# Optimization experiments

Hardware: AMD Instinct MI355X
Metric: run time of the kernel (lower is better)

Reference implementation:

```python
import jax, jax.numpy as jnp
import numpy as np

B, T, D, H = 4, 2048, 512, 8
DH = D // H  # 64
EPS = 1e-5


def setup_inputs() -> dict:
    key = jax.random.key(0)
    ks = jax.random.split(key, 12)
    s = lambda k, shp, fan: jax.random.normal(k, shp, jnp.float32) * (fan ** -0.5)
    return {
        "x": jax.random.normal(ks[0], (B, T, D), jnp.float32),
        "ln1_g": jnp.ones((D,), jnp.float32),
        "ln1_b": jnp.zeros((D,), jnp.float32),
        "Wq": s(ks[1], (H, D, DH), D),  # per-head bias-free projections
        "Wk": s(ks[2], (H, D, DH), D),
        "Wv": s(ks[3], (H, D, DH), D),
        "Wproj": s(ks[4], (D, D), D),
        "bproj": jnp.zeros((D,), jnp.float32),
        "W1": s(ks[5], (D, 4 * D), D),
        "b1": jnp.zeros((4 * D,), jnp.float32),
        "W2": s(ks[6], (4 * D, D), 4 * D),
        "b2": jnp.zeros((D,), jnp.float32),
    }


def _layernorm(x, g, b):
    m = jnp.mean(x, axis=-1, keepdims=True)
    v = jnp.var(x, axis=-1, keepdims=True)
    return (x - m) * jax.lax.rsqrt(v + EPS) * g + b


def reference(x, ln1_g, ln1_b, Wq, Wk, Wv, Wproj, bproj, W1, b1, W2, b2):
    b, t, c = x.shape
    scale = c ** -0.5  # source scales by input channel dim, not head_size
    causal = jnp.tril(jnp.ones((t, t), bool))  # [T,T]

    # --- attention sublayer (pre-norm with ln1) ---
    h = _layernorm(x, ln1_g, ln1_b)
    q = jnp.einsum('btd,hde->bhte', h, Wq)
    k = jnp.einsum('btd,hde->bhte', h, Wk)
    v = jnp.einsum('btd,hde->bhte', h, Wv)
    scores = jnp.einsum('bhte,bhse->bhts', q, k) * scale  # [B,H,T,T]
    scores = jnp.where(causal, scores, -jnp.inf)
    att = jax.nn.softmax(scores, axis=-1)  # dropout = identity at inference
    o = jnp.einsum('bhts,bhse->bthe', att, v).reshape(b, t, c)  # concat heads
    sa = o @ Wproj + bproj
    x = x + sa

    # --- FFN sublayer (source reuses ln1, faithful) ---
    h2 = _layernorm(x, ln1_g, ln1_b)
    ff = jax.nn.relu(h2 @ W1 + b1) @ W2 + b2
    return x + ff
```

## Files before the change

### kernel.cpp

```cpp
#include <hip/hip_runtime.h>
#include <math.h>

#define B_ 4
#define T_ 2048
#define D_ 512
#define H_ 8
#define DH_ 64
#define BT_ 8192
#define FF_ 2048
#define EPS_ 1e-5f
#define SCALE_ 0.04419417382415922f
#define SC2_ 0.06375861151f
#define NEGINF_ -1e30f

typedef short b16x8 __attribute__((ext_vector_type(8)));
typedef short b16x4 __attribute__((ext_vector_type(4)));
typedef float f32x4 __attribute__((ext_vector_type(4)));

#define MFMA16(a, b, c) __builtin_amdgcn_mfma_f32_16x16x32_bf16(a, b, c, 0, 0, 0)
#define MFMA16K16(a, b, c) __builtin_amdgcn_mfma_f32_16x16x16bf16_1k(a, b, c, 0, 0, 0)

#define GLL16(gp, lp) \
    __builtin_amdgcn_global_load_lds((const __attribute__((address_space(1))) void*)(gp), \
                                     (__attribute__((address_space(3))) void*)(lp), 16, 0, 0)

#if __has_builtin(__builtin_amdgcn_exp2f)
#define EXP2F(x) __builtin_amdgcn_exp2f(x)
#else
#define EXP2F(x) exp2f(x)
#endif

static __device__ inline short f2bf(float f) {
    unsigned int u = __builtin_bit_cast(unsigned int, f);
    unsigned int r = (u + 0x7fffu + ((u >> 16) & 1u)) >> 16;
    return (short)r;
}
static __device__ inline short f2bf_trunc(float f) {
    return (short)(__builtin_bit_cast(unsigned int, f) >> 16);
}

__global__ __launch_bounds__(64) void ln_kernel(const float* __restrict__ X,
        const float* __restrict__ G, const float* __restrict__ Bb,
        short* __restrict__ Y)
{
    int row = blockIdx.x;
    int t = threadIdx.x;
    const float* xr = X + (size_t)row * D_;
    float4 v0 = *(const float4*)(xr + t * 4);
    float4 v1 = *(const float4*)(xr + 256 + t * 4);
    float sum = v0.x + v0.y + v0.z + v0.w + v1.x + v1.y + v1.z + v1.w;
    float ssq = v0.x*v0.x + v0.y*v0.y + v0.z*v0.z + v0.w*v0.w
              + v1.x*v1.x + v1.y*v1.y + v1.z*v1.z + v1.w*v1.w;
    #pragma unroll
    for (int off = 32; off > 0; off >>= 1) {
        sum += __shfl_down(sum, off);
        ssq += __shfl_down(ssq, off);
    }
    sum = __shfl(sum, 0);
    ssq = __shfl(ssq, 0);
    float mean = sum * (1.0f / D_);
    float var  = ssq * (1.0f / D_) - mean * mean;
    float rstd = rsqrtf(var + EPS_);

    float4 g0 = *(const float4*)(G + t * 4);
    float4 g1 = *(const float4*)(G + 256 + t * 4);
    float4 b0 = *(const float4*)(Bb + t * 4);
    float4 b1 = *(const float4*)(Bb + 256 + t * 4);
    short4 o0, o1;
    o0.x = f2bf((v0.x - mean) * rstd * g0.x + b0.x);
    o0.y = f2bf((v0.y - mean) * rstd * g0.y + b0.y);
    o0.z = f2bf((v0.z - mean) * rstd * g0.z + b0.z);
    o0.w = f2bf((v0.w - mean) * rstd * g0.w + b0.w);
    o1.x = f2bf((v1.x - mean) * rstd * g1.x + b1.x);
    o1.y = f2bf((v1.y - mean) * rstd * g1.y + b1.y);
    o1.z = f2bf((v1.z - mean) * rstd * g1.z + b1.z);
    o1.w = f2bf((v1.w - mean) * rstd * g1.w + b1.w);
    short* yr = Y + (size_t)row * D_;
    *(short4*)(yr + t * 4)       = o0;
    *(short4*)(yr + 256 + t * 4) = o1;
}

__global__ __launch_bounds__(256) void prep_kernel(
        const float* __restrict__ Wq, const float* __restrict__ Wk,
        const float* __restrict__ Wv, const float* __restrict__ Wp,
        const float* __restrict__ W1, const float* __restrict__ W2,
        short* __restrict__ wqkv, short* __restrict__ wpt,
        short* __restrict__ w1t, short* __restrict__ w2t)
{
    __shared__ float tile[32][33];
    int idx = blockIdx.x;
    const float* src; short* dst; int R, C, tx0, ty0;
    if (idx < 768) {
        int w = idx >> 8, rem = idx & 255;
        int hh = rem >> 5, t = rem & 31;
        const float* base = (w == 0) ? Wq : ((w == 1) ? Wk : Wv);
        src = base + hh * (D_ * DH_);
        dst = wqkv + w * (512 * 512) + hh * (DH_ * D_);
        R = 512; C = 64; tx0 = (t & 1) * 32; ty0 = (t >> 1) * 32;
    } else if (idx < 1024) {
        int t = idx - 768;
        src = Wp; dst = wpt; R = 512; C = 512;
        tx0 = (t & 15) * 32; ty0 = (t >> 4) * 32;
    } else if (idx < 2048) {
        int t = idx - 1024;
        src = W1; dst = w1t; R = 512; C = 2048;
        tx0 = (t & 63) * 32; ty0 = (t >> 6) * 32;
    } else {
        int t = idx - 2048;
        src = W2; dst = w2t; R = 2048; C = 512;
        tx0 = (t & 15) * 32; ty0 = (t >> 4) * 32;
    }
    int tx = threadIdx.x, ty = threadIdx.y;
    #pragma unroll
    for (int i = 0; i < 32; i += 8)
        tile[ty + i][tx] = src[(size_t)(ty0 + ty + i) * C + tx0 + tx];
    __syncthreads();
    #pragma unroll
    for (int i = 0; i < 32; i += 8)
        dst[(size_t)(tx0 + ty + i) * R + ty0 + tx] = f2bf(tile[tx][ty + i]);
}

__global__ __launch_bounds__(256) void mm_kernel(const short* __restrict__ A,
        const short* __restrict__ Bt, void* __restrict__ C,
        const float* __restrict__ bias, const float* __restrict__ resid,
        int M, int N, int K, int relu, int out_bf16)
{
    __shared__ short As[2][128 * 32];
    __shared__ short Bs[2][128 * 32];
    const int tid = threadIdx.x;
    const int wave = tid >> 6, lane = tid & 63;
    const int quad = lane >> 4, l15 = lane & 15;
    const int m0 = blockIdx.x * 128, n0 = blockIdx.y * 128;
    const int mw = (wave & 1) * 64, nw = (wave >> 1) * 64;

#define STAGE_MM(bufi, kk) \
    { \
        for (int r = 0; r < 2; ++r) { \
            int c = r * 256 + tid; \
            int row = c >> 2, seg = (c & 3) ^ (row & 3); \
            GLL16(A + (size_t)(m0 + row) * K + (kk) + seg * 8, \
                  As[bufi] + (size_t)(r * 256 + wave * 64) * 8); \
            GLL16(Bt + (size_t)(n0 + row) * K + (kk) + seg * 8, \
                  Bs[bufi] + (size_t)(r * 256 + wave * 64) * 8); \
        } \
    }

    f32x4 acc[4][4];
    #pragma unroll
    for (int i = 0; i < 4; ++i)
        #pragma unroll
        for (int j = 0; j < 4; ++j)
            acc[i][j] = (f32x4){0.f, 0.f, 0.f, 0.f};

    STAGE_MM(0, 0);
    int buf = 0;
    for (int k0 = 0; k0 < K; k0 += 32) {
        __syncthreads();
        if (k0 + 32 < K) STAGE_MM(buf ^ 1, k0 + 32);
        b16x8 af[4], bf[4];
        #pragma unroll
        for (int i = 0; i < 4; ++i) {
            int row = mw + i * 16 + l15;
            af[i] = *(const b16x8*)(As[buf] + row * 32 + ((quad ^ (row & 3)) * 8));
        }
        #pragma unroll
        for (int j = 0; j < 4; ++j) {
            int row = nw + j * 16 + l15;
            bf[j] = *(const b16x8*)(Bs[buf] + row * 32 + ((quad ^ (row & 3)) * 8));
        }
        #pragma unroll
        for (int i = 0; i < 4; ++i)
            #pragma unroll
            for (int j = 0; j < 4; ++j)
                acc[i][j] = MFMA16(af[i], bf[j], acc[i][j]);
        buf ^= 1;
    }
#undef STAGE_MM

    #pragma unroll
    for (int i = 0; i < 4; ++i) {
        #pragma unroll
        for (int r = 0; r < 4; ++r) {
            size_t row = (size_t)(m0 + mw + i * 16 + quad * 4 + r);
            #pragma unroll
            for (int j = 0; j < 4; ++j) {
                int col = n0 + nw + j * 16 + l15;
                float v = acc[i][j][r];
                if (bias)  v += bias[col];
                if (resid) v += resid[row * N + col];
                if (relu)  v = fmaxf(v, 0.0f);
                if (out_bf16) ((short*)C)[row * N + col] = f2bf(v);
                else          ((float*)C)[row * N + col] = v;
            }
        }
    }
}

__global__ __launch_bounds__(256) void mm64_kernel(const short* __restrict__ A,
        const short* __restrict__ Bt, void* __restrict__ C,
        const float* __restrict__ bias, const float* __restrict__ resid,
        int M, int N, int K, int relu, int out_bf16)
{
    __shared__ short As[2][128 * 32];
    __shared__ short Bs[2][64 * 32];
    const int tid = threadIdx.x;
    const int wave = tid >> 6, lane = tid & 63;
    const int quad = lane >> 4, l15 = lane & 15;
    const int m0 = blockIdx.x * 128, n0 = blockIdx.y * 64;
    const int mw = (wave & 1) * 64, nw = (wave >> 1) * 32;

#define STAGE_M64(bufi, kk) \
    { \
        for (int r = 0; r < 2; ++r) { \
            int c = r * 256 + tid; \
            int row = c >> 2, seg = (c & 3) ^ (row & 3); \
            GLL16(A + (size_t)(m0 + row) * K + (kk) + seg * 8, \
                  As[bufi] + (size_t)(r * 256 + wave * 64) * 8); \
        } \
        { \
            int row = tid >> 2, seg = (tid & 3) ^ (row & 3); \
            GLL16(Bt + (size_t)(n0 + row) * K + (kk) + seg * 8, \
                  Bs[bufi] + (size_t)(wave * 64) * 8); \
        } \
    }

    f32x4 acc[4][2];
    #pragma unroll
    for (int i = 0; i < 4; ++i)
        #pragma unroll
        for (int j = 0; j < 2; ++j)
            acc[i][j] = (f32x4){0.f, 0.f, 0.f, 0.f};

    STAGE_M64(0, 0);
    int buf = 0;
    for (int k0 = 0; k0 < K; k0 += 32) {
        __syncthreads();
        if (k0 + 32 < K) STAGE_M64(buf ^ 1, k0 + 32);
        b16x8 af[4], bf[2];
        #pragma unroll
        for (int i = 0; i < 4; ++i) {
            int row = mw + i * 16 + l15;
            af[i] = *(const b16x8*)(As[buf] + row * 32 + ((quad ^ (row & 3)) * 8));
        }
        #pragma unroll
        for (int j = 0; j < 2; ++j) {
            int row = nw + j * 16 + l15;
            bf[j] = *(const b16x8*)(Bs[buf] + row * 32 + ((quad ^ (row & 3)) * 8));
        }
        #pragma unroll
        for (int i = 0; i < 4; ++i)
            #pragma unroll
            for (int j = 0; j < 2; ++j)
                acc[i][j] = MFMA16(af[i], bf[j], acc[i][j]);
        buf ^= 1;
    }
#undef STAGE_M64

    #pragma unroll
    for (int i = 0; i < 4; ++i) {
        #pragma unroll
        for (int r = 0; r < 4; ++r) {
            size_t row = (size_t)(m0 + mw + i * 16 + quad * 4 + r);
            #pragma unroll
            for (int j = 0; j < 2; ++j) {
                int col = n0 + nw + j * 16 + l15;
                float v = acc[i][j][r];
                if (bias)  v += bias[col];
                if (resid) v += resid[row * N + col];
                if (relu)  v = fmaxf(v, 0.0f);
                if (out_bf16) ((short*)C)[row * N + col] = f2bf(v);
                else          ((float*)C)[row * N + col] = v;
            }
        }
    }
}

__global__ __launch_bounds__(256) void mm6464_kernel(const short* __restrict__ A,
        const short* __restrict__ Bt, void* __restrict__ C,
        const float* __restrict__ bias, const float* __restrict__ resid,
        int M, int N, int K, int relu, int out_bf16)
{
    __shared__ short As[2][64 * 32];
    __shared__ short Bs[2][64 * 32];
    const int tid = threadIdx.x;
    const int wave = tid >> 6, lane = tid & 63;
    const int quad = lane >> 4, l15 = lane & 15;
    const int m0 = blockIdx.x * 64, n0 = blockIdx.y * 64;
    const int nw = wave * 16;

#define STAGE_M66(bufi, kk) \
    { \
        int row = tid >> 2, seg = (tid & 3) ^ (row & 3); \
        GLL16(A + (size_t)(m0 + row) * K + (kk) + seg * 8, \
              As[bufi] + (size_t)(wave * 64) * 8); \
        GLL16(Bt + (size_t)(n0 + row) * K + (kk) + seg * 8, \
              Bs[bufi] + (size_t)(wave * 64) * 8); \
    }

    f32x4 acc[4];
    #pragma unroll
    for (int i = 0; i < 4; ++i) acc[i] = (f32x4){0.f, 0.f, 0.f, 0.f};

    STAGE_M66(0, 0);
    int buf = 0;
    for (int k0 = 0; k0 < K; k0 += 32) {
        __syncthreads();
        if (k0 + 32 < K) STAGE_M66(buf ^ 1, k0 + 32);
        b16x8 af[4], bf;
        #pragma unroll
        for (int i = 0; i < 4; ++i) {
            int row = i * 16 + l15;
            af[i] = *(const b16x8*)(As[buf] + row * 32 + ((quad ^ (row & 3)) * 8));
        }
        {
            int row = nw + l15;
            bf = *(const b16x8*)(Bs[buf] + row * 32 + ((quad ^ (row & 3)) * 8));
        }
        #pragma unroll
        for (int i = 0; i < 4; ++i)
            acc[i] = MFMA16(af[i], bf, acc[i]);
        buf ^= 1;
    }
#undef STAGE_M66

    #pragma unroll
    for (int i = 0; i < 4; ++i) {
        #pragma unroll
        for (int r = 0; r < 4; ++r) {
            size_t row = (size_t)(m0 + i * 16 + quad * 4 + r);
            int col = n0 + nw + l15;
            float v = acc[i][r];
            if (bias)  v += bias[col];
            if (resid) v += resid[row * N + col];
            if (relu)  v = fmaxf(v, 0.0f);
            if (out_bf16) ((short*)C)[row * N + col] = f2bf(v);
            else          ((float*)C)[row * N + col] = v;
        }
    }
}

__global__ __launch_bounds__(256) void attn_kernel(const short* __restrict__ qkv,
        short* __restrict__ Ob)
{
    __shared__ short Qs[64 * 64];
    __shared__ short Ks[64 * 64];
    __shared__ short Vt[64 * 64];
    __shared__ short Osh[64 * 72];

    const int tid = threadIdx.x;
    const int wave = tid >> 6, lane = tid & 63;
    const int quad = lane >> 4, l15 = lane & 15;
    const int bh = blockIdx.x;
    const int qi = 31 - (int)blockIdx.y;
    const int b = bh >> 3, h = bh & 7;
    const size_t tok0 = (size_t)b * T_;
    const int qrow_rel = wave * 16 + l15;

    #pragma unroll
    for (int r = 0; r < 2; ++r) {
        int c = r * 256 + tid;
        int tk = c >> 3;
        int seg = (c & 7) ^ (tk & 7);
        GLL16(qkv + (tok0 + qi * 64 + tk) * 1536 + h * 64 + seg * 8,
              Qs + (size_t)(r * 256 + wave * 64) * 8);
    }

    float mrow = NEGINF_, lrow = 0.0f;
    f32x4 ot[4];
    #pragma unroll
    for (int dt = 0; dt < 4; ++dt) ot[dt] = (f32x4){0.f, 0.f, 0.f, 0.f};

    b16x8 qf[2];

    for (int kj = 0; kj <= qi; ++kj) {
        __syncthreads();
        #pragma unroll
        for (int r = 0; r < 2; ++r) {
            int c = r * 256 + tid;
            int tk = c >> 3;
            int seg = (c & 7) ^ (tk & 7);
            GLL16(qkv + (tok0 + kj * 64 + tk) * 1536 + 512 + h * 64 + seg * 8,
                  Ks + (size_t)(r * 256 + wave * 64) * 8);
        }
        {
            int s = tid >> 5, tp = tid & 31;
            const short* g0 = qkv + (tok0 + kj * 64 + tp * 2) * 1536 + 1024 + h * 64 + s * 8;
            b16x8 v0 = *(const b16x8*)g0;
            b16x8 v1 = *(const b16x8*)(g0 + 1536);
            int* vo = (int*)Vt;
            int gg = tp >> 1, half = tp & 1;
            #pragma unroll
            for (int e = 0; e < 8; ++e) {
                int row = s * 8 + e;
                unsigned int pk = (unsigned int)(unsigned short)v0[e]
                                | ((unsigned int)(unsigned short)v1[e] << 16);
                vo[row * 32 + ((gg ^ (row & 15)) << 1) + half] = pk;
            }
        }
        __syncthreads();

        if (kj == 0) {
            #pragma unroll
            for (int kb = 0; kb < 2; ++kb) {
                int row = wave * 16 + l15;
                qf[kb] = *(const b16x8*)(Qs + row * 64 + (((kb * 4 + quad) ^ (row & 7)) * 8));
            }
        }

        f32x4 st[4];
        #pragma unroll
        for (int mt = 0; mt < 4; ++mt) st[mt] = (f32x4){0.f, 0.f, 0.f, 0.f};
        #pragma unroll
        for (int mt = 0; mt < 4; ++mt) {
            int trow = mt * 16 + l15;
            #pragma unroll
            for (int kb = 0; kb < 2; ++kb) {
                b16x8 kf = *(const b16x8*)(Ks + trow * 64 + (((kb * 4 + quad) ^ (trow & 7)) * 8));
                st[mt] = MFMA16(kf, qf[kb], st[mt]);
            }
        }

        const bool diag = (kj == qi);
        float mx = NEGINF_;
        #pragma unroll
        for (int mt = 0; mt < 4; ++mt)
            #pragma unroll
            for (int r = 0; r < 4; ++r) {
                if (diag && (mt * 16 + quad * 4 + r) > qrow_rel) st[mt][r] = NEGINF_;
                mx = fmaxf(mx, st[mt][r]);
            }
        mx = fmaxf(mx, __shfl_xor(mx, 16));
        mx = fmaxf(mx, __shfl_xor(mx, 32));
        float mn = fmaxf(mrow, mx);
        float alpha = EXP2F((mrow - mn) * SC2_);
        float mnsc = mn * SC2_;
        mrow = mn;
        float rs = 0.0f;
        b16x4 pf[4];
        #pragma unroll
        for (int mt = 0; mt < 4; ++mt)
            #pragma unroll
            for (int r = 0; r < 4; ++r) {
                float e = EXP2F(fmaf(st[mt][r], SC2_, -mnsc));
                rs += e;
                pf[mt][r] = f2bf_trunc(e);
            }
        rs += __shfl_xor(rs, 16);
        rs += __shfl_xor(rs, 32);
        lrow = lrow * alpha + rs;
        #pragma unroll
        for (int dt = 0; dt < 4; ++dt) {
            ot[dt][0] *= alpha; ot[dt][1] *= alpha;
            ot[dt][2] *= alpha; ot[dt][3] *= alpha;
        }
        #pragma unroll
        for (int dt = 0; dt < 4; ++dt) {
            const short* vrow = Vt + (dt * 16 + l15) * 64;
            #pragma unroll
            for (int kt = 0; kt < 4; ++kt) {
                b16x4 vf = *(const b16x4*)(vrow + (((kt * 4 + quad) ^ l15) << 2));
                ot[dt] = MFMA16K16(vf, pf[kt], ot[dt]);
            }
        }
    }

    float inv = 1.0f / lrow;
    #pragma unroll
    for (int dt = 0; dt < 4; ++dt) {
        b16x4 o4;
        o4[0] = f2bf(ot[dt][0] * inv);
        o4[1] = f2bf(ot[dt][1] * inv);
        o4[2] = f2bf(ot[dt][2] * inv);
        o4[3] = f2bf(ot[dt][3] * inv);
        *(b16x4*)(Osh + (size_t)qrow_rel * 72 + dt * 16 + quad * 4) = o4;
    }
    {
        int row = tid >> 2, ch = tid & 3;
        b16x8 lo = *(const b16x8*)(Osh + (size_t)row * 72 + ch * 16);
        b16x8 hi = *(const b16x8*)(Osh + (size_t)row * 72 + ch * 16 + 8);
        short* dst = Ob + (tok0 + (size_t)qi * 64 + row) * 512 + h * 64 + ch * 16;
        *(b16x8*)dst = lo;
        *(b16x8*)(dst + 8) = hi;
    }
}

extern "C" void kernel_launch(void* const* d_in, const int* in_sizes, int n_in,
                              void* d_out, int out_size, void* d_ws, size_t ws_size,
                              hipStream_t stream) {
    (void)in_sizes; (void)n_in; (void)out_size; (void)ws_size;
    const float* x     = (const float*)d_in[0];
    const float* ln_g  = (const float*)d_in[1];
    const float* ln_b  = (const float*)d_in[2];
    const float* Wq    = (const float*)d_in[3];
    const float* Wk    = (const float*)d_in[4];
    const float* Wv    = (const float*)d_in[5];
    const float* Wproj = (const float*)d_in[6];
    const float* bproj = (const float*)d_in[7];
    const float* W1    = (const float*)d_in[8];
    const float* b1    = (const float*)d_in[9];
    const float* W2    = (const float*)d_in[10];
    const float* b2    = (const float*)d_in[11];
    float* out = (float*)d_out;

    char* W = (char*)d_ws;
    short* hbuf  = (short*)(W + 0);
    short* qkvb  = (short*)(W + ((size_t)8  << 20));
    short* attno = (short*)(W + ((size_t)32 << 20));
    float* x1    = (float*)(W + ((size_t)40 << 20));
    short* ff1   = (short*)(W + ((size_t)56 << 20));
    short* wqkv  = (short*)(W + ((size_t)88 << 20));
    short* wpt   = (short*)(W + ((size_t)90 << 20));
    short* w1t   = (short*)(W + ((size_t)91 << 20));
    short* w2t   = (short*)(W + ((size_t)93 << 20));

    prep_kernel<<<dim3(3072), dim3(32, 8), 0, stream>>>(
        Wq, Wk, Wv, Wproj, W1, W2, wqkv, wpt, w1t, w2t);
    ln_kernel<<<dim3(BT_), dim3(64), 0, stream>>>(x, ln_g, ln_b, hbuf);
    mm_kernel<<<dim3(64, 12), dim3(256), 0, stream>>>(hbuf, wqkv, qkvb,
        nullptr, nullptr, BT_, 1536, D_, 0, 1);
    attn_kernel<<<dim3(32, 32), dim3(256), 0, stream>>>(qkvb, attno);
    mm6464_kernel<<<dim3(128, 8), dim3(256), 0, stream>>>(attno, wpt, x1,
        bproj, x, BT_, D_, D_, 0, 0);
    ln_kernel<<<dim3(BT_), dim3(64), 0, stream>>>(x1, ln_g, ln_b, hbuf);
    mm_kernel<<<dim3(64, 16), dim3(256), 0, stream>>>(hbuf, w1t, ff1,
        b1, nullptr, BT_, FF_, D_, 1, 1);
    mm64_kernel<<<dim3(64, 8), dim3(256), 0, stream>>>(ff1, w2t, out,
        b2, x1, BT_, D_, FF_, 0, 0);
}
```

Before: 294.5 us.

## Split attention KV range in two and merge partials in a combine kernel

The attention kernel now splits each query tile's causal key range into two halves across a new grid dimension. Each half writes a normalized bf16 partial output and per-row max/sum to workspace, and a new combine kernel merges the two with log-sum-exp weights. This targets load imbalance and low block count from the triangular causal loop. In exchange it adds an extra launch, extra global traffic for the partials, and an additional bf16 rounding of the partial outputs.

```diff
diff --git a/kernel.cpp b/kernel.cpp
--- a/kernel.cpp
+++ b/kernel.cpp
@@ -37,6 +37,9 @@
 }
 static __device__ inline short f2bf_trunc(float f) {
     return (short)(__builtin_bit_cast(unsigned int, f) >> 16);
+}
+static __device__ inline float bf2f(short s) {
+    return __builtin_bit_cast(float, ((unsigned int)(unsigned short)s) << 16);
 }
 
 __global__ __launch_bounds__(64) void ln_kernel(const float* __restrict__ X,
@@ -340,21 +343,33 @@
 }
 
 __global__ __launch_bounds__(256) void attn_kernel(const short* __restrict__ qkv,
-        short* __restrict__ Ob)
-{
-    __shared__ short Qs[64 * 64];
+        short* __restrict__ Opart, float* __restrict__ Ml)
+{
+    __shared__ short Qs[64 * 72];
     __shared__ short Ks[64 * 64];
     __shared__ short Vt[64 * 64];
-    __shared__ short Osh[64 * 72];
 
     const int tid = threadIdx.x;
     const int wave = tid >> 6, lane = tid & 63;
     const int quad = lane >> 4, l15 = lane & 15;
     const int bh = blockIdx.x;
     const int qi = 31 - (int)blockIdx.y;
+    const int split = blockIdx.z;
     const int b = bh >> 3, h = bh & 7;
     const size_t tok0 = (size_t)b * T_;
     const int qrow_rel = wave * 16 + l15;
+    const int half = (qi + 1) >> 1;
+    const int klo = split ? half : 0;
+    const int khi = split ? qi + 1 : half;
+    const int pidx = split * 1024 + bh * 32 + qi;
+    short* Op = Opart + (size_t)pidx * 4096;
+    float* mlp = Ml + (size_t)pidx * 128;
+
+    if (klo >= khi) {
+        for (int i = tid; i < 2048; i += 256) ((int*)Op)[i] = 0;
+        if (tid < 64) { mlp[tid] = NEGINF_; mlp[64 + tid] = 0.0f; }
+        return;
+    }
 
     #pragma unroll
     for (int r = 0; r < 2; ++r) {
@@ -372,7 +387,7 @@
 
     b16x8 qf[2];
 
-    for (int kj = 0; kj <= qi; ++kj) {
+    for (int kj = klo; kj < khi; ++kj) {
         __syncthreads();
         #pragma unroll
         for (int r = 0; r < 2; ++r) {
@@ -388,18 +403,18 @@
             b16x8 v0 = *(const b16x8*)g0;
             b16x8 v1 = *(const b16x8*)(g0 + 1536);
             int* vo = (int*)Vt;
-            int gg = tp >> 1, half = tp & 1;
+            int gg = tp >> 1, hlf = tp & 1;
             #pragma unroll
             for (int e = 0; e < 8; ++e) {
                 int row = s * 8 + e;
                 unsigned int pk = (unsigned int)(unsigned short)v0[e]
                                 | ((unsigned int)(unsigned short)v1[e] << 16);
-                vo[row * 32 + ((gg ^ (row & 15)) << 1) + half] = pk;
+                vo[row * 32 + ((gg ^ (row & 15)) << 1) + hlf] = pk;
             }
         }
         __syncthreads();
 
-        if (kj == 0) {
+        if (kj == klo) {
             #pragma unroll
             for (int kb = 0; kb < 2; ++kb) {
                 int row = wave * 16 + l15;
@@ -464,6 +479,7 @@
         }
     }
 
+    __syncthreads();
     float inv = 1.0f / lrow;
     #pragma unroll
     for (int dt = 0; dt < 4; ++dt) {
@@ -472,15 +488,53 @@
         o4[1] = f2bf(ot[dt][1] * inv);
         o4[2] = f2bf(ot[dt][2] * inv);
         o4[3] = f2bf(ot[dt][3] * inv);
-        *(b16x4*)(Osh + (size_t)qrow_rel * 72 + dt * 16 + quad * 4) = o4;
+        *(b16x4*)(Qs + (size_t)qrow_rel * 72 + dt * 16 + quad * 4) = o4;
     }
     {
         int row = tid >> 2, ch = tid & 3;
-        b16x8 lo = *(const b16x8*)(Osh + (size_t)row * 72 + ch * 16);
-        b16x8 hi = *(const b16x8*)(Osh + (size_t)row * 72 + ch * 16 + 8);
-        short* dst = Ob + (tok0 + (size_t)qi * 64 + row) * 512 + h * 64 + ch * 16;
+        b16x8 lo = *(const b16x8*)(Qs + (size_t)row * 72 + ch * 16);
+        b16x8 hi = *(const b16x8*)(Qs + (size_t)row * 72 + ch * 16 + 8);
+        short* dst = Op + row * 64 + ch * 16;
         *(b16x8*)dst = lo;
         *(b16x8*)(dst + 8) = hi;
+    }
+    if (quad == 0) {
+        mlp[qrow_rel] = mrow;
+        mlp[64 + qrow_rel] = lrow;
+    }
+}
+
+__global__ __launch_bounds__(256) void attn_combine_kernel(
+        const short* __restrict__ Opart, const float* __restrict__ Ml,
+        short* __restrict__ Ob)
+{
+    int pair = blockIdx.x;
+    int bh = pair >> 5, qi = pair & 31;
+    int b = bh >> 3, h = bh & 7;
+    int tid = threadIdx.x;
+    const short* O1 = Opart + (size_t)pair * 4096;
+    const short* O2 = Opart + (size_t)(1024 + pair) * 4096;
+    const float* ml1 = Ml + (size_t)pair * 128;
+    const float* ml2 = Ml + (size_t)(1024 + pair) * 128;
+    int ch = tid & 7;
+    #pragma unroll
+    for (int it = 0; it < 2; ++it) {
+        int row = it * 32 + (tid >> 3);
+        float m1 = ml1[row], l1 = ml1[64 + row];
+        float m2 = ml2[row], l2 = ml2[64 + row];
+        float mx = fmaxf(m1, m2);
+        float e1 = l1 * EXP2F((m1 - mx) * SC2_);
+        float e2 = l2 * EXP2F((m2 - mx) * SC2_);
+        float inv = 1.0f / (e1 + e2);
+        float w1 = e1 * inv, w2 = e2 * inv;
+        b16x8 a = *(const b16x8*)(O1 + row * 64 + ch * 8);
+        b16x8 c = *(const b16x8*)(O2 + row * 64 + ch * 8);
+        b16x8 o;
+        #pragma unroll
+        for (int e = 0; e < 8; ++e)
+            o[e] = f2bf(w1 * bf2f(a[e]) + w2 * bf2f(c[e]));
+        short* dst = Ob + ((size_t)(b * T_ + qi * 64 + row)) * 512 + h * 64 + ch * 8;
+        *(b16x8*)dst = o;
     }
 }
 
@@ -512,13 +566,16 @@
     short* wpt   = (short*)(W + ((size_t)90 << 20));
     short* w1t   = (short*)(W + ((size_t)91 << 20));
     short* w2t   = (short*)(W + ((size_t)93 << 20));
+    short* Opart = (short*)(W + ((size_t)56 << 20));
+    float* Ml    = (float*)(W + ((size_t)72 << 20));
 
     prep_kernel<<<dim3(3072), dim3(32, 8), 0, stream>>>(
         Wq, Wk, Wv, Wproj, W1, W2, wqkv, wpt, w1t, w2t);
     ln_kernel<<<dim3(BT_), dim3(64), 0, stream>>>(x, ln_g, ln_b, hbuf);
     mm_kernel<<<dim3(64, 12), dim3(256), 0, stream>>>(hbuf, wqkv, qkvb,
         nullptr, nullptr, BT_, 1536, D_, 0, 1);
-    attn_kernel<<<dim3(32, 32), dim3(256), 0, stream>>>(qkvb, attno);
+    attn_kernel<<<dim3(32, 32, 2), dim3(256), 0, stream>>>(qkvb, Opart, Ml);
+    attn_combine_kernel<<<dim3(1024), dim3(256), 0, stream>>>(Opart, Ml, attno);
     mm6464_kernel<<<dim3(128, 8), dim3(256), 0, stream>>>(attno, wpt, x1,
         bproj, x, BT_, D_, D_, 0, 0);
     ln_kernel<<<dim3(BT_), dim3(64), 0, stream>>>(x1, ln_g, ln_b, hbuf);
```

Measured after the change: 289.6 us. No clear change (-1.7%).
